# Performance work log

Hardware: AMD Instinct MI355X
Metric: run time of the kernel (lower is better)

Reference implementation:

```python
import jax, jax.numpy as jnp
import numpy as np
import math

B, T, VOCAB, RANK = 32, 1024, 512, 256


def setup_inputs() -> dict:
    key = jax.random.key(0)
    k1, k2, k3, k4, k5 = jax.random.split(key, 5)
    scale_attn = 1.0 / math.sqrt(VOCAB)
    scale_proj = 1.0 / math.sqrt(RANK)
    return {
        "x": jax.random.normal(k1, (B, T, VOCAB), dtype=jnp.float32),
        "W_attn": jax.random.normal(k2, (VOCAB, 3 * RANK), dtype=jnp.float32) * scale_attn,
        "b_attn": jax.random.normal(k3, (3 * RANK,), dtype=jnp.float32) * 0.01,
        "W_proj": jax.random.normal(k4, (RANK, VOCAB), dtype=jnp.float32) * scale_proj,
        "b_proj": jax.random.normal(k5, (VOCAB,), dtype=jnp.float32) * 0.01,
    }


def reference(x, W_attn, b_attn, W_proj, b_proj):
    # x: [B, T, vocab]
    Bb, Tt, _ = x.shape
    qkv = x @ W_attn + b_attn              # [B, T, 3*rank]
    q, k, v = jnp.split(qkv, 3, axis=-1)   # each [B, T, rank]
    scale = 1.0 / math.sqrt(k.shape[-1])
    att = jnp.einsum('btd,bsd->bts', q, k) * scale  # [B, T, T]
    # causal mask (masked=True)
    mask = jnp.tril(jnp.ones((Tt, Tt), dtype=bool))
    att = jnp.where(mask[None, :, :], att, -jnp.inf)
    att = jax.nn.softmax(att, axis=-1)
    # dropout layers are identity in eval mode (p=0 attn, p=0.1 resid disabled)
    y = jnp.einsum('bts,bsd->btd', att, v)  # [B, T, rank]
    y = y @ W_proj + b_proj                 # [B, T, vocab]
    return jax.nn.gelu(y, approximate=False)
```

## Files before the change

kernel.cpp:

```cpp
#include <hip/hip_runtime.h>
#include <hip/hip_bf16.h>
#include <math.h>

typedef __bf16 bf16;
typedef __attribute__((ext_vector_type(8))) __bf16 bf16x8;
typedef __attribute__((ext_vector_type(4))) __bf16 bf16x4;
typedef __attribute__((ext_vector_type(4))) float f32x4;

#define MFMA16(a, b, c) __builtin_amdgcn_mfma_f32_16x16x32_bf16((a), (b), (c), 0, 0, 0)


__global__ __launch_bounds__(256) void cvt_wattn(const float* __restrict__ w,
                                                 bf16* __restrict__ wt) {
  int o = blockIdx.x * 256 + threadIdx.x;
  int n = o >> 9, kk = o & 511;
  wt[o] = (bf16)w[kk * 768 + n];
}

__global__ __launch_bounds__(256) void cvt_wproj(const float* __restrict__ w,
                                                 bf16* __restrict__ wt) {
  int o = blockIdx.x * 256 + threadIdx.x;
  int n = o >> 8, kk = o & 255;
  wt[o] = (bf16)w[kk * 512 + n];
}

__global__ __launch_bounds__(256) void gemm_qkv(
    const float* __restrict__ x, const bf16* __restrict__ WT,
    const float* __restrict__ b_attn,
    bf16* __restrict__ qo, bf16* __restrict__ ko, bf16* __restrict__ vo) {
  __shared__ __attribute__((aligned(16))) bf16 As[128][40];
  __shared__ __attribute__((aligned(16))) bf16 Bs[128][40];
  const int tid = threadIdx.x;
  const int id = blockIdx.x;
  const int xcd = id & 7;
  const int rest = id >> 3;
  const int bmL = rest / 6;
  const int bn = (rest % 6) * 128;
  const int bm = (xcd * 32 + bmL) * 128;
  const int lane = tid & 63, wid = tid >> 6;
  const int l15 = lane & 15, lg = lane >> 4;
  const int wm = (wid >> 1) * 64, wn = (wid & 1) * 64;

  f32x4 acc[4][4] = {};

  const int srow = tid >> 1;
  const int scol = (tid & 1) * 16;
  const float* xp = x + (size_t)(bm + srow) * 512 + scol;
  const bf16* wp = WT + (size_t)(bn + srow) * 512 + scol;

  bf16x8 ha[2], hb[2];
  {
    f32x4 f0 = *(const f32x4*)(xp);
    f32x4 f1 = *(const f32x4*)(xp + 4);
    f32x4 f2 = *(const f32x4*)(xp + 8);
    f32x4 f3 = *(const f32x4*)(xp + 12);
#pragma unroll
    for (int e = 0; e < 4; ++e) {
      ha[0][e] = (bf16)f0[e]; ha[0][e + 4] = (bf16)f1[e];
      ha[1][e] = (bf16)f2[e]; ha[1][e + 4] = (bf16)f3[e];
    }
    hb[0] = *(const bf16x8*)(wp);
    hb[1] = *(const bf16x8*)(wp + 8);
  }

  for (int kt = 0; kt < 16; ++kt) {
    __syncthreads();
    *(bf16x8*)&As[srow][scol] = ha[0];
    *(bf16x8*)&As[srow][scol + 8] = ha[1];
    *(bf16x8*)&Bs[srow][scol] = hb[0];
    *(bf16x8*)&Bs[srow][scol + 8] = hb[1];
    __syncthreads();
    if (kt < 15) {
      f32x4 f0 = *(const f32x4*)(xp + (kt + 1) * 32);
      f32x4 f1 = *(const f32x4*)(xp + (kt + 1) * 32 + 4);
      f32x4 f2 = *(const f32x4*)(xp + (kt + 1) * 32 + 8);
      f32x4 f3 = *(const f32x4*)(xp + (kt + 1) * 32 + 12);
#pragma unroll
      for (int e = 0; e < 4; ++e) {
        ha[0][e] = (bf16)f0[e]; ha[0][e + 4] = (bf16)f1[e];
        ha[1][e] = (bf16)f2[e]; ha[1][e + 4] = (bf16)f3[e];
      }
      hb[0] = *(const bf16x8*)(wp + (kt + 1) * 32);
      hb[1] = *(const bf16x8*)(wp + (kt + 1) * 32 + 8);
    }
    bf16x8 af[4], bfr[4];
#pragma unroll
    for (int mi = 0; mi < 4; ++mi)
      af[mi] = *(const bf16x8*)&As[wm + mi * 16 + l15][lg * 8];
#pragma unroll
    for (int ni = 0; ni < 4; ++ni)
      bfr[ni] = *(const bf16x8*)&Bs[wn + ni * 16 + l15][lg * 8];
    __builtin_amdgcn_s_setprio(1);
#pragma unroll
    for (int mi = 0; mi < 4; ++mi)
#pragma unroll
      for (int ni = 0; ni < 4; ++ni)
        acc[mi][ni] = MFMA16(bfr[ni], af[mi], acc[mi][ni]);
    __builtin_amdgcn_s_setprio(0);
  }

#pragma unroll
  for (int ni = 0; ni < 4; ++ni) {
    int gc0 = bn + wn + ni * 16 + lg * 4;
    f32x4 bias = *(const f32x4*)(b_attn + gc0);
    int seg = gc0 >> 8;
    int cc = gc0 & 255;
    bf16* op = (seg == 0) ? qo : ((seg == 1) ? ko : vo);
#pragma unroll
    for (int mi = 0; mi < 4; ++mi) {
      int gr = bm + wm + mi * 16 + l15;
      bf16x4 pk;
#pragma unroll
      for (int r = 0; r < 4; ++r) pk[r] = (bf16)(acc[mi][ni][r] + bias[r]);
      *(bf16x4*)(op + (size_t)gr * 256 + cc) = pk;
    }
  }
}

__global__ __launch_bounds__(256) void transpose_v(const bf16* __restrict__ v,
                                                   bf16* __restrict__ vt) {
  __shared__ bf16 tile[32][33];
  const int b = blockIdx.z;
  const int t0 = blockIdx.x * 32;
  const int d0 = blockIdx.y * 32;
  const int tid = threadIdx.x;
  const int r = tid >> 3, c4 = (tid & 7) * 4;
  bf16x4 in = *(const bf16x4*)(v + (size_t)(b * 1024 + t0 + r) * 256 + d0 + c4);
  tile[r][c4] = in[0]; tile[r][c4 + 1] = in[1];
  tile[r][c4 + 2] = in[2]; tile[r][c4 + 3] = in[3];
  __syncthreads();
  bf16x4 o;
  o[0] = tile[c4][r]; o[1] = tile[c4 + 1][r];
  o[2] = tile[c4 + 2][r]; o[3] = tile[c4 + 3][r];
  *(bf16x4*)(vt + (size_t)(b * 256 + d0 + r) * 1024 + t0 + c4) = o;
}

__global__ __launch_bounds__(512) void attn_fwd(
    const bf16* __restrict__ q, const bf16* __restrict__ k,
    const bf16* __restrict__ vt, bf16* __restrict__ y) {
  __shared__ __attribute__((aligned(16))) bf16 Ks[64][264];
  __shared__ __attribute__((aligned(16))) bf16 Vt[256][72];
  __shared__ __attribute__((aligned(16))) bf16 Ps[8][16][72];
  const int tid = threadIdx.x, lane = tid & 63, wid = tid >> 6;
  const int l15 = lane & 15, lg = lane >> 4;

  const int id = blockIdx.x;
  const int xcd = id & 7;
  const int rest = id >> 3;
  const int qt = rest & 7;
  const int bg = rest >> 3;
  const int b = xcd + 8 * bg;
  const int q0 = qt * 128 + wid * 16;

  bf16x8 qf[8];
  {
    const bf16* qp = q + (size_t)(b * 1024 + q0 + l15) * 256 + lg * 8;
#pragma unroll
    for (int d = 0; d < 8; ++d) qf[d] = *(const bf16x8*)(qp + d * 32);
  }
  f32x4 o[16] = {};
  float m_st = -1e30f;
  float l_st = 0.f;

  const bf16* kbase = k + (size_t)b * 1024 * 256;
  const bf16* vtbase = vt + (size_t)b * 256 * 1024;
  const int ksr = tid >> 5, ksc = (tid & 31) * 8;
  const int vsr = tid >> 3, vsc = (tid & 7) * 8;

  const int ntiles = 2 * qt + 2;

  bf16x8 kreg[4], vreg[4];
#pragma unroll
  for (int i = 0; i < 4; ++i)
    kreg[i] = *(const bf16x8*)(kbase + (size_t)(ksr + i * 16) * 256 + ksc);
#pragma unroll
  for (int i = 0; i < 4; ++i)
    vreg[i] = *(const bf16x8*)(vtbase + (size_t)(vsr + i * 64) * 1024 + vsc);

  for (int tt = 0; tt < ntiles; ++tt) {
    const int kv0 = tt * 64;
    __syncthreads();
#pragma unroll
    for (int i = 0; i < 4; ++i)
      *(bf16x8*)&Ks[ksr + i * 16][ksc] = kreg[i];
#pragma unroll
    for (int i = 0; i < 4; ++i)
      *(bf16x8*)&Vt[vsr + i * 64][vsc] = vreg[i];
    __syncthreads();
    if (tt + 1 < ntiles) {
      const bf16* kp = kbase + (size_t)(kv0 + 64 + ksr) * 256 + ksc;
      const bf16* vp = vtbase + (size_t)vsr * 1024 + kv0 + 64 + vsc;
#pragma unroll
      for (int i = 0; i < 4; ++i)
        kreg[i] = *(const bf16x8*)(kp + (size_t)i * 16 * 256);
#pragma unroll
      for (int i = 0; i < 4; ++i)
        vreg[i] = *(const bf16x8*)(vp + (size_t)i * 64 * 1024);
    }

    f32x4 st[4] = {};
    __builtin_amdgcn_s_setprio(1);
#pragma unroll
    for (int nf = 0; nf < 4; ++nf)
#pragma unroll
      for (int dc = 0; dc < 8; ++dc) {
        bf16x8 kb = *(const bf16x8*)&Ks[nf * 16 + l15][dc * 32 + lg * 8];
        st[nf] = MFMA16(kb, qf[dc], st[nf]);
      }
    __builtin_amdgcn_s_setprio(0);

    const int qg = q0 + l15;
    float tmax = -1e30f;
#pragma unroll
    for (int nf = 0; nf < 4; ++nf)
#pragma unroll
      for (int r = 0; r < 4; ++r) {
        int sg = kv0 + nf * 16 + lg * 4 + r;
        float v = st[nf][r] * 0.0625f;
        v = (sg > qg) ? -1e30f : v;
        st[nf][r] = v;
        tmax = fmaxf(tmax, v);
      }
    tmax = fmaxf(tmax, __shfl_xor(tmax, 16, 64));
    tmax = fmaxf(tmax, __shfl_xor(tmax, 32, 64));

    if (!__all(tmax <= m_st + 8.f)) {
      float mnew = fmaxf(m_st, tmax);
      float corr = __expf(m_st - mnew);
      m_st = mnew;
      l_st *= corr;
#pragma unroll
      for (int df = 0; df < 16; ++df)
#pragma unroll
        for (int r = 0; r < 4; ++r) o[df][r] *= corr;
    }

    float rsum = 0.f;
#pragma unroll
    for (int nf = 0; nf < 4; ++nf) {
      bf16x4 pk;
#pragma unroll
      for (int r = 0; r < 4; ++r) {
        float p = __expf(st[nf][r] - m_st);
        rsum += p;
        pk[r] = (bf16)p;
      }
      *(bf16x4*)&Ps[wid][l15][nf * 16 + lg * 4] = pk;
    }
    rsum += __shfl_xor(rsum, 16, 64);
    rsum += __shfl_xor(rsum, 32, 64);
    l_st += rsum;

    bf16x8 pa0 = *(const bf16x8*)&Ps[wid][l15][lg * 8];
    bf16x8 pa1 = *(const bf16x8*)&Ps[wid][l15][32 + lg * 8];
    __builtin_amdgcn_s_setprio(1);
#pragma unroll
    for (int df = 0; df < 16; ++df) {
      bf16x8 vb0 = *(const bf16x8*)&Vt[df * 16 + l15][lg * 8];
      bf16x8 vb1 = *(const bf16x8*)&Vt[df * 16 + l15][32 + lg * 8];
      o[df] = MFMA16(vb0, pa0, o[df]);
      o[df] = MFMA16(vb1, pa1, o[df]);
    }
    __builtin_amdgcn_s_setprio(0);
  }

  float inv = 1.f / l_st;
  bf16* yp = y + (size_t)(b * 1024 + q0 + l15) * 256 + lg * 4;
#pragma unroll
  for (int df = 0; df < 16; ++df) {
    bf16x4 pk;
#pragma unroll
    for (int r = 0; r < 4; ++r) pk[r] = (bf16)(o[df][r] * inv);
    *(bf16x4*)(yp + df * 16) = pk;
  }
}

__global__ __launch_bounds__(256) void gemm_proj(
    const bf16* __restrict__ y, const bf16* __restrict__ WT,
    const float* __restrict__ b_proj, float* __restrict__ out) {
  __shared__ __attribute__((aligned(16))) bf16 As[128][40];
  __shared__ __attribute__((aligned(16))) bf16 Bs[128][40];
  const int tid = threadIdx.x;
  const int id = blockIdx.x;
  const int xcd = id & 7;
  const int rest = id >> 3;
  const int bmL = rest >> 2;
  const int bn = (rest & 3) * 128;
  const int bm = (xcd * 32 + bmL) * 128;
  const int lane = tid & 63, wid = tid >> 6;
  const int l15 = lane & 15, lg = lane >> 4;
  const int wm = (wid >> 1) * 64, wn = (wid & 1) * 64;
  f32x4 acc[4][4] = {};

  const int srow = tid >> 1, scol = (tid & 1) * 16;
  const bf16* yp = y + (size_t)(bm + srow) * 256 + scol;
  const bf16* wp = WT + (size_t)(bn + srow) * 256 + scol;

  bf16x8 ha[2], hb[2];
  ha[0] = *(const bf16x8*)(yp);
  ha[1] = *(const bf16x8*)(yp + 8);
  hb[0] = *(const bf16x8*)(wp);
  hb[1] = *(const bf16x8*)(wp + 8);

  for (int kt = 0; kt < 8; ++kt) {
    __syncthreads();
    *(bf16x8*)&As[srow][scol] = ha[0];  *(bf16x8*)&As[srow][scol + 8] = ha[1];
    *(bf16x8*)&Bs[srow][scol] = hb[0];  *(bf16x8*)&Bs[srow][scol + 8] = hb[1];
    __syncthreads();
    if (kt < 7) {
      ha[0] = *(const bf16x8*)(yp + (kt + 1) * 32);
      ha[1] = *(const bf16x8*)(yp + (kt + 1) * 32 + 8);
      hb[0] = *(const bf16x8*)(wp + (kt + 1) * 32);
      hb[1] = *(const bf16x8*)(wp + (kt + 1) * 32 + 8);
    }
    bf16x8 af[4], bfr[4];
#pragma unroll
    for (int mi = 0; mi < 4; ++mi)
      af[mi] = *(const bf16x8*)&As[wm + mi * 16 + l15][lg * 8];
#pragma unroll
    for (int ni = 0; ni < 4; ++ni)
      bfr[ni] = *(const bf16x8*)&Bs[wn + ni * 16 + l15][lg * 8];
    __builtin_amdgcn_s_setprio(1);
#pragma unroll
    for (int mi = 0; mi < 4; ++mi)
#pragma unroll
      for (int ni = 0; ni < 4; ++ni)
        acc[mi][ni] = MFMA16(bfr[ni], af[mi], acc[mi][ni]);
    __builtin_amdgcn_s_setprio(0);
  }

#pragma unroll
  for (int ni = 0; ni < 4; ++ni) {
    int gc0 = bn + wn + ni * 16 + lg * 4;
    f32x4 bias = *(const f32x4*)(b_proj + gc0);
#pragma unroll
    for (int mi = 0; mi < 4; ++mi) {
      int gr = bm + wm + mi * 16 + l15;
      f32x4 g;
#pragma unroll
      for (int r = 0; r < 4; ++r) {
        float v = acc[mi][ni][r] + bias[r];
        float z = 1.5957691216f * (v + 0.044715f * v * v * v);
        float t = __expf(z);
        float th = 1.f - 2.f / (t + 1.f);
        g[r] = 0.5f * v * (1.f + th);
      }
      *(f32x4*)(out + (size_t)gr * 512 + gc0) = g;
    }
  }
}

extern "C" void kernel_launch(void* const* d_in, const int* in_sizes, int n_in,
                              void* d_out, int out_size, void* d_ws, size_t ws_size,
                              hipStream_t stream) {
  const float* x      = (const float*)d_in[0];
  const float* W_attn = (const float*)d_in[1];
  const float* b_attn = (const float*)d_in[2];
  const float* W_proj = (const float*)d_in[3];
  const float* b_proj = (const float*)d_in[4];
  float* out = (float*)d_out;
  char* ws = (char*)d_ws;

  const size_t SZ = 16777216;
  bf16* WT1 = (bf16*)(ws);
  bf16* WT2 = (bf16*)(ws + 786432);
  bf16* qb  = (bf16*)(ws + 1048576);
  bf16* kb  = (bf16*)(ws + 1048576 + SZ);
  bf16* vb  = (bf16*)(ws + 1048576 + 2 * SZ);
  bf16* vtb = (bf16*)(ws + 1048576 + 3 * SZ);
  bf16* yb  = vb;

  cvt_wattn<<<dim3(1536), dim3(256), 0, stream>>>(W_attn, WT1);
  cvt_wproj<<<dim3(512), dim3(256), 0, stream>>>(W_proj, WT2);
  gemm_qkv<<<dim3(1536), dim3(256), 0, stream>>>(x, WT1, b_attn, qb, kb, vb);
  transpose_v<<<dim3(32, 8, 32), dim3(256), 0, stream>>>(vb, vtb);
  attn_fwd<<<dim3(256), dim3(512), 0, stream>>>(qb, kb, vtb, yb);
  gemm_proj<<<dim3(1024), dim3(256), 0, stream>>>(yb, WT2, b_proj, out);
}
```

Before: 153.6 us.

## Fuse V transpose into QKV epilogue, swizzle attention LDS, rebalance causal tiles

The QKV GEMM epilogue now writes V directly in transposed [B, D, T] layout, which removes the separate transpose kernel and one round trip of V through memory. The attention kernel moves to 256-thread blocks, each covering 64 query rows across 512 blocks. Query tiles are paired (j and 23-j) so that causal work is balanced across blocks. Padded LDS arrays are replaced by XOR-swizzled layouts to avoid bank conflicts without the padding. The risk is that the transposed V stores are scattered 2-byte writes, which may coalesce poorly.

```diff
diff --git a/kernel.cpp b/kernel.cpp
--- a/kernel.cpp
+++ b/kernel.cpp
@@ -27,7 +27,7 @@
 __global__ __launch_bounds__(256) void gemm_qkv(
     const float* __restrict__ x, const bf16* __restrict__ WT,
     const float* __restrict__ b_attn,
-    bf16* __restrict__ qo, bf16* __restrict__ ko, bf16* __restrict__ vo) {
+    bf16* __restrict__ qo, bf16* __restrict__ ko, bf16* __restrict__ vto) {
   __shared__ __attribute__((aligned(16))) bf16 As[128][40];
   __shared__ __attribute__((aligned(16))) bf16 Bs[128][40];
   const int tid = threadIdx.x;
@@ -105,52 +105,44 @@
     f32x4 bias = *(const f32x4*)(b_attn + gc0);
     int seg = gc0 >> 8;
     int cc = gc0 & 255;
-    bf16* op = (seg == 0) ? qo : ((seg == 1) ? ko : vo);
-#pragma unroll
-    for (int mi = 0; mi < 4; ++mi) {
-      int gr = bm + wm + mi * 16 + l15;
-      bf16x4 pk;
-#pragma unroll
-      for (int r = 0; r < 4; ++r) pk[r] = (bf16)(acc[mi][ni][r] + bias[r]);
-      *(bf16x4*)(op + (size_t)gr * 256 + cc) = pk;
-    }
-  }
-}
-
-__global__ __launch_bounds__(256) void transpose_v(const bf16* __restrict__ v,
-                                                   bf16* __restrict__ vt) {
-  __shared__ bf16 tile[32][33];
-  const int b = blockIdx.z;
-  const int t0 = blockIdx.x * 32;
-  const int d0 = blockIdx.y * 32;
-  const int tid = threadIdx.x;
-  const int r = tid >> 3, c4 = (tid & 7) * 4;
-  bf16x4 in = *(const bf16x4*)(v + (size_t)(b * 1024 + t0 + r) * 256 + d0 + c4);
-  tile[r][c4] = in[0]; tile[r][c4 + 1] = in[1];
-  tile[r][c4 + 2] = in[2]; tile[r][c4 + 3] = in[3];
-  __syncthreads();
-  bf16x4 o;
-  o[0] = tile[c4][r]; o[1] = tile[c4 + 1][r];
-  o[2] = tile[c4 + 2][r]; o[3] = tile[c4 + 3][r];
-  *(bf16x4*)(vt + (size_t)(b * 256 + d0 + r) * 1024 + t0 + c4) = o;
-}
-
-__global__ __launch_bounds__(512) void attn_fwd(
+    if (seg == 2) {
+#pragma unroll
+      for (int mi = 0; mi < 4; ++mi) {
+        int gr = bm + wm + mi * 16 + l15;
+        bf16* vp = vto + (size_t)(gr >> 10) * 262144 + (size_t)cc * 1024 + (gr & 1023);
+#pragma unroll
+        for (int r = 0; r < 4; ++r)
+          vp[(size_t)r * 1024] = (bf16)(acc[mi][ni][r] + bias[r]);
+      }
+    } else {
+      bf16* op = (seg == 0) ? qo : ko;
+#pragma unroll
+      for (int mi = 0; mi < 4; ++mi) {
+        int gr = bm + wm + mi * 16 + l15;
+        bf16x4 pk;
+#pragma unroll
+        for (int r = 0; r < 4; ++r) pk[r] = (bf16)(acc[mi][ni][r] + bias[r]);
+        *(bf16x4*)(op + (size_t)gr * 256 + cc) = pk;
+      }
+    }
+  }
+}
+
+__global__ __launch_bounds__(256) void attn_fwd(
     const bf16* __restrict__ q, const bf16* __restrict__ k,
     const bf16* __restrict__ vt, bf16* __restrict__ y) {
-  __shared__ __attribute__((aligned(16))) bf16 Ks[64][264];
-  __shared__ __attribute__((aligned(16))) bf16 Vt[256][72];
-  __shared__ __attribute__((aligned(16))) bf16 Ps[8][16][72];
+  __shared__ __attribute__((aligned(16))) bf16 Ks[64 * 256];
+  __shared__ __attribute__((aligned(16))) bf16 Vt[256 * 64];
+  __shared__ __attribute__((aligned(16))) bf16 Ps[4 * 16 * 64];
   const int tid = threadIdx.x, lane = tid & 63, wid = tid >> 6;
   const int l15 = lane & 15, lg = lane >> 4;
 
   const int id = blockIdx.x;
-  const int xcd = id & 7;
-  const int rest = id >> 3;
-  const int qt = rest & 7;
-  const int bg = rest >> 3;
+  const int xcd = id & 7, u = id >> 3;
+  const int bg = u & 3, j = u >> 2;
   const int b = xcd + 8 * bg;
-  const int q0 = qt * 128 + wid * 16;
+  const int qt = (j < 8) ? j : 23 - j;
+  const int q0 = qt * 64 + wid * 16;
 
   bf16x8 qf[8];
   {
@@ -162,51 +154,58 @@
   float m_st = -1e30f;
   float l_st = 0.f;
 
-  const bf16* kbase = k + (size_t)b * 1024 * 256;
-  const bf16* vtbase = vt + (size_t)b * 256 * 1024;
-  const int ksr = tid >> 5, ksc = (tid & 31) * 8;
-  const int vsr = tid >> 3, vsc = (tid & 7) * 8;
-
-  const int ntiles = 2 * qt + 2;
-
-  bf16x8 kreg[4], vreg[4];
-#pragma unroll
-  for (int i = 0; i < 4; ++i)
-    kreg[i] = *(const bf16x8*)(kbase + (size_t)(ksr + i * 16) * 256 + ksc);
-#pragma unroll
-  for (int i = 0; i < 4; ++i)
-    vreg[i] = *(const bf16x8*)(vtbase + (size_t)(vsr + i * 64) * 1024 + vsc);
+  const char* kbase = (const char*)(k + (size_t)b * 262144);
+  const char* vtbase = (const char*)(vt + (size_t)b * 262144);
+  const int ksr = tid >> 5;
+  const int kscb = (tid & 31) * 16;
+  const int kkey = ksr << 4;
+  const int vsr = tid >> 3;
+  const int vscb = (tid & 7) * 16;
+  const int vkey = (vsr & 7) << 4;
+  const int rkey = (l15 & 7) << 4;
+
+  const int ntiles = qt + 1;
+
+  bf16x8 kreg[8], vreg[8];
+#pragma unroll
+  for (int i = 0; i < 8; ++i)
+    kreg[i] = *(const bf16x8*)(kbase + (size_t)(ksr + i * 8) * 512 + kscb);
+#pragma unroll
+  for (int i = 0; i < 8; ++i)
+    vreg[i] = *(const bf16x8*)(vtbase + (size_t)(vsr + i * 32) * 2048 + vscb);
 
   for (int tt = 0; tt < ntiles; ++tt) {
     const int kv0 = tt * 64;
     __syncthreads();
 #pragma unroll
-    for (int i = 0; i < 4; ++i)
-      *(bf16x8*)&Ks[ksr + i * 16][ksc] = kreg[i];
-#pragma unroll
-    for (int i = 0; i < 4; ++i)
-      *(bf16x8*)&Vt[vsr + i * 64][vsc] = vreg[i];
+    for (int i = 0; i < 8; ++i)
+      *(bf16x8*)((char*)Ks + (size_t)(ksr + i * 8) * 512 + (kscb ^ kkey)) = kreg[i];
+#pragma unroll
+    for (int i = 0; i < 8; ++i)
+      *(bf16x8*)((char*)Vt + (size_t)(vsr + i * 32) * 128 + (vscb ^ vkey)) = vreg[i];
     __syncthreads();
     if (tt + 1 < ntiles) {
-      const bf16* kp = kbase + (size_t)(kv0 + 64 + ksr) * 256 + ksc;
-      const bf16* vp = vtbase + (size_t)vsr * 1024 + kv0 + 64 + vsc;
-#pragma unroll
-      for (int i = 0; i < 4; ++i)
-        kreg[i] = *(const bf16x8*)(kp + (size_t)i * 16 * 256);
-#pragma unroll
-      for (int i = 0; i < 4; ++i)
-        vreg[i] = *(const bf16x8*)(vp + (size_t)i * 64 * 1024);
+      const char* kp = kbase + (size_t)(kv0 + 64) * 512;
+      const char* vp = vtbase + (size_t)(kv0 + 64) * 2;
+#pragma unroll
+      for (int i = 0; i < 8; ++i)
+        kreg[i] = *(const bf16x8*)(kp + (size_t)(ksr + i * 8) * 512 + kscb);
+#pragma unroll
+      for (int i = 0; i < 8; ++i)
+        vreg[i] = *(const bf16x8*)(vp + (size_t)(vsr + i * 32) * 2048 + vscb);
     }
 
     f32x4 st[4] = {};
     __builtin_amdgcn_s_setprio(1);
 #pragma unroll
-    for (int nf = 0; nf < 4; ++nf)
+    for (int nf = 0; nf < 4; ++nf) {
+      const char* rp = (const char*)Ks + (size_t)(nf * 16 + l15) * 512;
 #pragma unroll
       for (int dc = 0; dc < 8; ++dc) {
-        bf16x8 kb = *(const bf16x8*)&Ks[nf * 16 + l15][dc * 32 + lg * 8];
+        bf16x8 kb = *(const bf16x8*)(rp + ((dc * 64 + lg * 16) ^ rkey));
         st[nf] = MFMA16(kb, qf[dc], st[nf]);
       }
+    }
     __builtin_amdgcn_s_setprio(0);
 
     const int qg = q0 + l15;
@@ -235,6 +234,7 @@
         for (int r = 0; r < 4; ++r) o[df][r] *= corr;
     }
 
+    char* psw = (char*)Ps + wid * 2048 + l15 * 128;
     float rsum = 0.f;
 #pragma unroll
     for (int nf = 0; nf < 4; ++nf) {
@@ -245,19 +245,20 @@
         rsum += p;
         pk[r] = (bf16)p;
       }
-      *(bf16x4*)&Ps[wid][l15][nf * 16 + lg * 4] = pk;
+      *(bf16x4*)(psw + ((nf * 32 + lg * 8) ^ rkey)) = pk;
     }
     rsum += __shfl_xor(rsum, 16, 64);
     rsum += __shfl_xor(rsum, 32, 64);
     l_st += rsum;
 
-    bf16x8 pa0 = *(const bf16x8*)&Ps[wid][l15][lg * 8];
-    bf16x8 pa1 = *(const bf16x8*)&Ps[wid][l15][32 + lg * 8];
+    bf16x8 pa0 = *(const bf16x8*)(psw + ((lg * 16) ^ rkey));
+    bf16x8 pa1 = *(const bf16x8*)(psw + ((64 + lg * 16) ^ rkey));
     __builtin_amdgcn_s_setprio(1);
 #pragma unroll
     for (int df = 0; df < 16; ++df) {
-      bf16x8 vb0 = *(const bf16x8*)&Vt[df * 16 + l15][lg * 8];
-      bf16x8 vb1 = *(const bf16x8*)&Vt[df * 16 + l15][32 + lg * 8];
+      const char* rp = (const char*)Vt + (size_t)(df * 16 + l15) * 128;
+      bf16x8 vb0 = *(const bf16x8*)(rp + ((lg * 16) ^ rkey));
+      bf16x8 vb1 = *(const bf16x8*)(rp + ((64 + lg * 16) ^ rkey));
       o[df] = MFMA16(vb0, pa0, o[df]);
       o[df] = MFMA16(vb1, pa1, o[df]);
     }
@@ -366,14 +367,12 @@
   bf16* WT2 = (bf16*)(ws + 786432);
   bf16* qb  = (bf16*)(ws + 1048576);
   bf16* kb  = (bf16*)(ws + 1048576 + SZ);
-  bf16* vb  = (bf16*)(ws + 1048576 + 2 * SZ);
-  bf16* vtb = (bf16*)(ws + 1048576 + 3 * SZ);
-  bf16* yb  = vb;
+  bf16* vtb = (bf16*)(ws + 1048576 + 2 * SZ);
+  bf16* yb  = (bf16*)(ws + 1048576 + 3 * SZ);
 
   cvt_wattn<<<dim3(1536), dim3(256), 0, stream>>>(W_attn, WT1);
   cvt_wproj<<<dim3(512), dim3(256), 0, stream>>>(W_proj, WT2);
-  gemm_qkv<<<dim3(1536), dim3(256), 0, stream>>>(x, WT1, b_attn, qb, kb, vb);
-  transpose_v<<<dim3(32, 8, 32), dim3(256), 0, stream>>>(vb, vtb);
-  attn_fwd<<<dim3(256), dim3(512), 0, stream>>>(qb, kb, vtb, yb);
+  gemm_qkv<<<dim3(1536), dim3(256), 0, stream>>>(x, WT1, b_attn, qb, kb, vtb);
+  attn_fwd<<<dim3(512), dim3(256), 0, stream>>>(qb, kb, vtb, yb);
   gemm_proj<<<dim3(1024), dim3(256), 0, stream>>>(yb, WT2, b_proj, out);
 }
```

New measurement: 135.2 us. 12.0% less time.
